# Performance work log

Measured on AMD Instinct MI355X. Metric: run time of the kernel, lower is better.

Reference implementation:

```python
import jax, jax.numpy as jnp
import numpy as np

K = 8
WRM = 40


def _gru(x, h, w_ih, w_hh, b_ih, b_hh):
    # PyTorch GRU cell: gates ordered (r, z, n)
    gi = x @ w_ih.T + b_ih
    gh = h @ w_hh.T + b_hh
    i_r, i_z, i_n = jnp.split(gi, 3, axis=-1)
    h_r, h_z, h_n = jnp.split(gh, 3, axis=-1)
    r = jax.nn.sigmoid(i_r + h_r)
    z = jax.nn.sigmoid(i_z + h_z)
    n = jnp.tanh(i_n + r * h_n)
    return (1.0 - z) * n + z * h


def setup_inputs() -> dict:
    key = jax.random.key(0)
    ks = jax.random.split(key, 20)
    T, B, C, Wd, H = 240, 64, 1, 84, 84
    N, M, E, A = 512, 256, 32, 18
    D = C * Wd * H
    u = lambda k, s, sc: jax.random.uniform(k, s, jnp.float32, -sc, sc)
    sM = float(1.0 / np.sqrt(M))
    sD = float(1.0 / np.sqrt(D))
    return dict(
        obs_seq=jax.random.normal(ks[0], (T, B, C, Wd, H), jnp.float32),
        act_seq=jax.random.randint(ks[1], (T, B), 0, A),
        w_enc=u(ks[2], (N, D), sD), b_enc=u(ks[3], (N,), sD),
        w_ih=u(ks[4], (3 * M, N), sM), w_hh=u(ks[5], (3 * M, M), sM),
        b_ih=u(ks[6], (3 * M,), sM), b_hh=u(ks[7], (3 * M,), sM),
        w_ih_c=u(ks[8], (3 * M, E), sM), w_hh_c=u(ks[9], (3 * M, M), sM),
        b_ih_c=u(ks[10], (3 * M,), sM), b_hh_c=u(ks[11], (3 * M,), sM),
        W1=u(ks[12], (M, M), sM), b1=u(ks[13], (M,), sM),
        W2=u(ks[14], (N, M), sM), b2=u(ks[15], (N,), sM),
        emb=jax.random.normal(ks[16], (A, E), jnp.float32),
    )


def reference(obs_seq, act_seq, w_enc, b_enc, w_ih, w_hh, b_ih, b_hh,
              w_ih_c, w_hh_c, b_ih_c, b_hh_c, W1, b1, W2, b2, emb):
    T, B = obs_seq.shape[0], obs_seq.shape[1]
    M = w_hh.shape[1]
    # encoder: flatten + linear -> (T, B, N)
    z = obs_seq.reshape(T, B, -1) @ w_enc.T + b_enc
    wrm_seq, trn_seq = z[:WRM], z[WRM:]
    acts = act_seq[WRM:]

    h0 = jnp.zeros((B, M), z.dtype)
    warm_hn, _ = jax.lax.scan(
        lambda h, x: (_gru(x, h, w_ih, w_hh, b_ih, b_hh), None), h0, wrm_seq)
    warm_hn = jax.lax.stop_gradient(warm_hn)  # torch.no_grad() warmup

    def cls_step(h, x):
        h2 = _gru(x, h, w_ih, w_hh, b_ih, b_hh)
        return h2, h2

    _, bts = jax.lax.scan(cls_step, warm_hn, trn_seq)  # (T', B, M)

    Tp = bts.shape[0]
    Tout = Tp - K
    idx = jnp.arange(Tout)[:, None] + jnp.arange(K)[None, :]  # (Tout, K)
    act_win = emb[acts[idx]]  # (Tout, K, B, E)

    def open_step(h, x):  # h: (Tout, B, M), x: (Tout, B, E)
        h2 = _gru(x, h, w_ih_c, w_hh_c, b_ih_c, b_hh_c)
        zt = jax.nn.relu(h2 @ W1.T + b1) @ W2.T + b2
        return h2, zt

    _, zs = jax.lax.scan(open_step, bts[:Tout], jnp.transpose(act_win, (1, 0, 2, 3)))
    return jnp.transpose(zs, (1, 0, 2, 3))  # (Tout, K, B, N)
```

## Files before the change

kernel.cpp:

```cpp
#include <hip/hip_runtime.h>
#include <hip/hip_fp16.h>
#include <math.h>

#define TT   240
#define BBATCH 64
#define DDIM 7056
#define KENC_PAD 7072
#define NENC 512
#define MHID 256
#define G3   768
#define WRMC 40
#define KWIN 8
#define TOUTC 192
#define RROWS (TOUTC*BBATCH)
#define NSTEPS (WRMC + TOUTC)

#define B_GI     ((size_t)0)
#define B_WENCH  ((size_t)0)
#define B_GBH    ((size_t)0)
#define B_R1H    ((size_t)37748736)
#define B_ZH     ((size_t)45613056)
#define B_HOPEN  ((size_t)45613056)
#define B_BTS    ((size_t)60817408)
#define B_BTSH   ((size_t)73400320)
#define B_HOPENH ((size_t)79691776)
#define B_WIHH   ((size_t)85983232)
#define B_WHHCH  ((size_t)86769664)
#define B_W1H    ((size_t)87162880)
#define B_W2H    ((size_t)87293952)
#define B_GTAB   ((size_t)87556096)
#define B_WT8    ((size_t)87611392)

typedef _Float16 half8 __attribute__((ext_vector_type(8)));
typedef _Float16 h2v  __attribute__((ext_vector_type(2)));
typedef __attribute__((ext_vector_type(4))) float f32x4;

__device__ __forceinline__ float sigmf(float x) { return 1.0f / (1.0f + expf(-x)); }
__device__ __forceinline__ h2v u2h2(unsigned int u) {
  union { unsigned int u; h2v h; } c; c.u = u; return c.h;
}

__global__ void wconv_kernel(const float* __restrict__ W, __half* __restrict__ o,
                             int N, int K, int Kpad) {
  const int idx = blockIdx.x * 256 + threadIdx.x;
  if (idx >= N * Kpad) return;
  const int n = idx / Kpad, k = idx % Kpad;
  o[idx] = __float2half((k < K) ? W[(size_t)n * K + k] : 0.f);
}

__global__ __launch_bounds__(256, 4) void gemm_h(
    const void* __restrict__ A, int a_fp32, const __half* __restrict__ W,
    const float* __restrict__ bias, void* __restrict__ C,
    int M, int N, int K, int Kpad, int relu, int out_h, int outk)
{
  __shared__ __half Ah[64][40];
  __shared__ __half Bh[256][40];
  const int tid = threadIdx.x;
  const int bx = blockIdx.x, by = blockIdx.y;
  const int w = tid >> 6;
  const int lane = tid & 63;
  const int l15 = lane & 15;
  const int khalf = (lane >> 4) * 8;

  f32x4 acc[4][4];
#pragma unroll
  for (int i = 0; i < 4; ++i)
#pragma unroll
    for (int j = 0; j < 4; ++j) acc[i][j] = (f32x4){0.f, 0.f, 0.f, 0.f};

  const int arow = tid >> 2;
  const int akq = (tid & 3) * 8;

  for (int k0 = 0; k0 < Kpad; k0 += 32) {
    __syncthreads();
    if (a_fp32) {
      const float* Af = (const float*)A;
      float4 v0 = make_float4(0.f, 0.f, 0.f, 0.f);
      float4 v1 = make_float4(0.f, 0.f, 0.f, 0.f);
      const size_t base = (size_t)(by * 64 + arow) * K + k0 + akq;
      if (k0 + akq < K)     v0 = *(const float4*)(Af + base);
      if (k0 + akq + 4 < K) v1 = *(const float4*)(Af + base + 4);
      __half2 hh[4];
      hh[0] = __floats2half2_rn(v0.x, v0.y);
      hh[1] = __floats2half2_rn(v0.z, v0.w);
      hh[2] = __floats2half2_rn(v1.x, v1.y);
      hh[3] = __floats2half2_rn(v1.z, v1.w);
      *(float4*)&Ah[arow][akq] = *(float4*)hh;
    } else {
      const __half* Ahp = (const __half*)A;
      *(float4*)&Ah[arow][akq] =
          *(const float4*)(Ahp + (size_t)(by * 64 + arow) * Kpad + k0 + akq);
    }
#pragma unroll
    for (int u = 0; u < 4; ++u) {
      const int f = tid + u * 256;
      const int n = f >> 2;
      const int kq8 = (f & 3) * 8;
      *(float4*)&Bh[n][kq8] =
          *(const float4*)(W + (size_t)(bx * 256 + n) * Kpad + k0 + kq8);
    }
    __syncthreads();

    half8 ah[4], bh[4];
#pragma unroll
    for (int i = 0; i < 4; ++i) {
      ah[i] = *(half8*)&Ah[i * 16 + l15][khalf];
      bh[i] = *(half8*)&Bh[w * 64 + i * 16 + l15][khalf];
    }
#pragma unroll
    for (int i = 0; i < 4; ++i)
#pragma unroll
      for (int j = 0; j < 4; ++j)
        acc[i][j] = __builtin_amdgcn_mfma_f32_16x16x32_f16(ah[i], bh[j], acc[i][j], 0, 0, 0);
  }

  const int r4 = (lane >> 4) * 4;
#pragma unroll
  for (int j = 0; j < 4; ++j) {
    const int col = bx * 256 + w * 64 + j * 16 + l15;
    const float bc = bias ? bias[col] : 0.f;
#pragma unroll
    for (int i = 0; i < 4; ++i) {
      const int mbase = by * 64 + i * 16 + r4;
#pragma unroll
      for (int r = 0; r < 4; ++r) {
        const int m = mbase + r;
        float vv = acc[i][j][r] + bc;
        if (relu) vv = fmaxf(vv, 0.f);
        if (outk >= 0) {
          const int t = m >> 6, b = m & 63;
          ((float*)C)[(((size_t)(t * KWIN + outk) * BBATCH + b) * NENC) + col] = vv;
        } else if (out_h) {
          ((__half*)C)[(size_t)m * N + col] = __float2half(vv);
        } else {
          ((float*)C)[(size_t)m * N + col] = vv;
        }
      }
    }
  }
}

__global__ void gitab_kernel(const float* __restrict__ emb, const float* __restrict__ w_ih_c,
                             const float* __restrict__ b_ih_c, float* __restrict__ gt)
{
  const int idx = blockIdx.x * blockDim.x + threadIdx.x;
  if (idx >= 18 * G3) return;
  const int a = idx / G3, cgate = idx % G3;
  float s = b_ih_c[cgate];
#pragma unroll
  for (int e = 0; e < 32; ++e) s = fmaf(emb[a * 32 + e], w_ih_c[cgate * 32 + e], s);
  gt[idx] = s;
}

__global__ void transpose_whh_p8(const float* __restrict__ w, float4* __restrict__ wt8) {
  const int id = blockIdx.x * 256 + threadIdx.x;
  if (id >= 32 * G3) return;
  const int k8 = id / G3, j = id % G3;
  const float* src = w + (size_t)j * MHID + k8 * 8;
  __half2 h2[4];
#pragma unroll
  for (int q = 0; q < 4; ++q)
    h2[q] = __floats2half2_rn(src[2 * q], src[2 * q + 1]);
  wt8[id] = *(float4*)h2;
}

__global__ __launch_bounds__(768, 3) void scan4_kernel(
    const float* __restrict__ gi_all, const float4* __restrict__ wt8,
    const float* __restrict__ b_hh, float* __restrict__ bts,
    __half* __restrict__ bts_h)
{
  const int b = blockIdx.x;
  const int j = threadIdx.x;
  __shared__ __align__(16) float hs[256];
  __shared__ __align__(16) __half hs16[256];
  __shared__ float gacc[768];

  unsigned int wreg[128];
#pragma unroll
  for (int k8 = 0; k8 < 32; ++k8) {
    const float4 v = wt8[(size_t)k8 * G3 + j];
    const uint4 u = *(const uint4*)&v;
    wreg[k8 * 4 + 0] = u.x; wreg[k8 * 4 + 1] = u.y;
    wreg[k8 * 4 + 2] = u.z; wreg[k8 * 4 + 3] = u.w;
  }
  const float bj = b_hh[j];
  if (j < 256) { hs[j] = 0.f; hs16[j] = __float2half(0.f); }
  __syncthreads();

  const uint4* h16v = (const uint4*)hs16;

  for (int t = 0; t < NSTEPS; ++t) {
    float gr = 0.f, gz = 0.f, gn = 0.f;
    if (j < 256) {
      const float* gp = gi_all + ((size_t)t * BBATCH + b) * G3;
      gr = gp[j]; gz = gp[256 + j]; gn = gp[512 + j];
    }

    float a0 = bj, a1 = 0.f, a2 = 0.f, a3 = 0.f;
#pragma unroll
    for (int k8 = 0; k8 < 32; ++k8) {
      const uint4 hu = h16v[k8];
#if __has_builtin(__builtin_amdgcn_fdot2)
      a0 = __builtin_amdgcn_fdot2(u2h2(wreg[k8 * 4 + 0]), u2h2(hu.x), a0, false);
      a1 = __builtin_amdgcn_fdot2(u2h2(wreg[k8 * 4 + 1]), u2h2(hu.y), a1, false);
      a2 = __builtin_amdgcn_fdot2(u2h2(wreg[k8 * 4 + 2]), u2h2(hu.z), a2, false);
      a3 = __builtin_amdgcn_fdot2(u2h2(wreg[k8 * 4 + 3]), u2h2(hu.w), a3, false);
#else
      {
        const h2v w0 = u2h2(wreg[k8 * 4 + 0]), w1 = u2h2(wreg[k8 * 4 + 1]);
        const h2v w2 = u2h2(wreg[k8 * 4 + 2]), w3 = u2h2(wreg[k8 * 4 + 3]);
        const h2v x0 = u2h2(hu.x), x1 = u2h2(hu.y), x2 = u2h2(hu.z), x3 = u2h2(hu.w);
        a0 = fmaf((float)w0.x, (float)x0.x, a0); a0 = fmaf((float)w0.y, (float)x0.y, a0);
        a1 = fmaf((float)w1.x, (float)x1.x, a1); a1 = fmaf((float)w1.y, (float)x1.y, a1);
        a2 = fmaf((float)w2.x, (float)x2.x, a2); a2 = fmaf((float)w2.y, (float)x2.y, a2);
        a3 = fmaf((float)w3.x, (float)x3.x, a3); a3 = fmaf((float)w3.y, (float)x3.y, a3);
      }
#endif
    }
    gacc[j] = (a0 + a1) + (a2 + a3);
    __syncthreads();

    if (j < 256) {
      const float r = sigmf(gr + gacc[j]);
      const float z = sigmf(gz + gacc[256 + j]);
      const float n = tanhf(gn + r * gacc[512 + j]);
      const float hn = (1.f - z) * n + z * hs[j];
      hs[j] = hn;
      hs16[j] = __float2half(hn);
      if (t >= WRMC) {
        const size_t o = (((size_t)(t - WRMC)) * BBATCH + b) * MHID + j;
        bts[o] = hn;
        bts_h[o] = __float2half(hn);
      }
    }
    __syncthreads();
  }
}

__global__ __launch_bounds__(256) void open_gates(
    const float* __restrict__ gtab, const int* __restrict__ act_seq,
    const float* __restrict__ gh, const float* __restrict__ hin,
    float* __restrict__ hout, __half* __restrict__ hout_h, int kstep)
{
  const int row = blockIdx.x;
  const int j = threadIdx.x;
  const int t = row >> 6, b = row & 63;
  const int a = act_seq[(WRMC + t + kstep) * BBATCH + b];
  const float* gi = gtab + a * G3;
  const float gr = gi[j], gz = gi[256 + j], gn = gi[512 + j];
  const size_t g0 = (size_t)row * G3;
  const float hr = gh[g0 + j], hz = gh[g0 + 256 + j], hnn = gh[g0 + 512 + j];
  const float h = hin[(size_t)row * MHID + j];
  const float r = sigmf(gr + hr);
  const float z = sigmf(gz + hz);
  const float n = tanhf(gn + r * hnn);
  const float hn = (1.f - z) * n + z * h;
  hout[(size_t)row * MHID + j] = hn;
  hout_h[(size_t)row * MHID + j] = __float2half(hn);
}

extern "C" void kernel_launch(void* const* d_in, const int* in_sizes, int n_in,
                              void* d_out, int out_size, void* d_ws, size_t ws_size,
                              hipStream_t stream) {
  const float* obs    = (const float*)d_in[0];
  const int*   act    = (const int*)  d_in[1];
  const float* w_enc  = (const float*)d_in[2];
  const float* b_enc  = (const float*)d_in[3];
  const float* w_ih   = (const float*)d_in[4];
  const float* w_hh   = (const float*)d_in[5];
  const float* b_ih   = (const float*)d_in[6];
  const float* b_hh   = (const float*)d_in[7];
  const float* w_ih_c = (const float*)d_in[8];
  const float* w_hh_c = (const float*)d_in[9];
  const float* b_ih_c = (const float*)d_in[10];
  const float* b_hh_c = (const float*)d_in[11];
  const float* W1     = (const float*)d_in[12];
  const float* b1     = (const float*)d_in[13];
  const float* W2     = (const float*)d_in[14];
  const float* b2     = (const float*)d_in[15];
  const float* emb    = (const float*)d_in[16];

  char* wsb = (char*)d_ws;
  float* out = (float*)d_out;

  float*  gi      = (float*)(wsb + B_GI);
  float*  gbh     = (float*)(wsb + B_GBH);
  __half* r1_h    = (__half*)(wsb + B_R1H);
  __half* z_h     = (__half*)(wsb + B_ZH);
  float*  hopen   = (float*)(wsb + B_HOPEN);
  float*  bts     = (float*)(wsb + B_BTS);
  __half* bts_h   = (__half*)(wsb + B_BTSH);
  __half* hopen_h = (__half*)(wsb + B_HOPENH);
  __half* enc_h   = (__half*)(wsb + B_WENCH);
  __half* ih_h    = (__half*)(wsb + B_WIHH);
  __half* hhc_h   = (__half*)(wsb + B_WHHCH);
  __half* w1_h    = (__half*)(wsb + B_W1H);
  __half* w2_h    = (__half*)(wsb + B_W2H);
  float*  gtab    = (float*)(wsb + B_GTAB);
  float4* wt8     = (float4*)(wsb + B_WT8);

  const dim3 blk(256);

  wconv_kernel<<<(NENC * KENC_PAD + 255) / 256, blk, 0, stream>>>(w_enc, enc_h, NENC, DDIM, KENC_PAD);
  wconv_kernel<<<(G3 * NENC + 255) / 256, blk, 0, stream>>>(w_ih, ih_h, G3, NENC, NENC);
  wconv_kernel<<<(G3 * MHID + 255) / 256, blk, 0, stream>>>(w_hh_c, hhc_h, G3, MHID, MHID);
  wconv_kernel<<<(MHID * MHID + 255) / 256, blk, 0, stream>>>(W1, w1_h, MHID, MHID, MHID);
  wconv_kernel<<<(NENC * MHID + 255) / 256, blk, 0, stream>>>(W2, w2_h, NENC, MHID, MHID);
  gitab_kernel<<<54, 256, 0, stream>>>(emb, w_ih_c, b_ih_c, gtab);
  transpose_whh_p8<<<(32 * G3 + 255) / 256, blk, 0, stream>>>(w_hh, wt8);

  gemm_h<<<dim3(NENC / 256, NSTEPS * BBATCH / 64), blk, 0, stream>>>(
      obs, 1, enc_h, b_enc, z_h, NSTEPS * BBATCH, NENC, DDIM, KENC_PAD, 0, 1, -1);
  gemm_h<<<dim3(G3 / 256, NSTEPS * BBATCH / 64), blk, 0, stream>>>(
      z_h, 0, ih_h, b_ih, gi, NSTEPS * BBATCH, G3, NENC, NENC, 0, 0, -1);

  scan4_kernel<<<BBATCH, 768, 0, stream>>>(gi, wt8, b_hh, bts, bts_h);

  for (int k = 0; k < KWIN; ++k) {
    const __half* hin_h = (k == 0) ? bts_h : hopen_h;
    const float*  hin   = (k == 0) ? bts   : hopen;
    gemm_h<<<dim3(G3 / 256, RROWS / 64), blk, 0, stream>>>(
        hin_h, 0, hhc_h, b_hh_c, gbh, RROWS, G3, MHID, MHID, 0, 0, -1);
    open_gates<<<RROWS, 256, 0, stream>>>(gtab, act, gbh, hin, hopen, hopen_h, k);
    gemm_h<<<dim3(MHID / 256, RROWS / 64), blk, 0, stream>>>(
        hopen_h, 0, w1_h, b1, r1_h, RROWS, MHID, MHID, MHID, 1, 1, -1);
    gemm_h<<<dim3(NENC / 256, RROWS / 64), blk, 0, stream>>>(
        r1_h, 0, w2_h, b2, out, RROWS, NENC, MHID, MHID, 0, 0, k);
  }
}
```

Before: 1.206 ms.

## Double-buffer GEMM tiles with register prefetch and halve N tile width

```diff
diff --git a/kernel.cpp b/kernel.cpp
--- a/kernel.cpp
+++ b/kernel.cpp
@@ -48,76 +48,90 @@
   o[idx] = __float2half((k < K) ? W[(size_t)n * K + k] : 0.f);
 }
 
-__global__ __launch_bounds__(256, 4) void gemm_h(
-    const void* __restrict__ A, int a_fp32, const __half* __restrict__ W,
+template<int AF32>
+__device__ __forceinline__ void load_tile(
+    const void* A, const __half* W, int by, int bx, int K, int Kpad,
+    int arow, int akq, int tid, int it,
+    float4& ra0, float4& ra1, float4& rah, float4& rb0, float4& rb1)
+{
+  const int k0 = it * 32;
+  if (AF32) {
+    const float* Af = (const float*)A;
+    ra0 = make_float4(0.f, 0.f, 0.f, 0.f); ra1 = ra0;
+    const size_t base = (size_t)(by * 64 + arow) * K + k0 + akq;
+    if (k0 + akq < K)     ra0 = *(const float4*)(Af + base);
+    if (k0 + akq + 4 < K) ra1 = *(const float4*)(Af + base + 4);
+  } else {
+    rah = *(const float4*)((const __half*)A + (size_t)(by * 64 + arow) * Kpad + k0 + akq);
+  }
+  const int bn = tid >> 2, bk = (tid & 3) * 8;
+  rb0 = *(const float4*)(W + (size_t)(bx * 128 + bn) * Kpad + k0 + bk);
+  rb1 = *(const float4*)(W + (size_t)(bx * 128 + 64 + bn) * Kpad + k0 + bk);
+}
+
+template<int AF32>
+__global__ __launch_bounds__(256, 4) void gemm_hp(
+    const void* __restrict__ A, const __half* __restrict__ W,
     const float* __restrict__ bias, void* __restrict__ C,
     int M, int N, int K, int Kpad, int relu, int out_h, int outk)
 {
-  __shared__ __half Ah[64][40];
-  __shared__ __half Bh[256][40];
+  __shared__ __half Ah[2][64][40];
+  __shared__ __half Bh[2][128][40];
   const int tid = threadIdx.x;
   const int bx = blockIdx.x, by = blockIdx.y;
   const int w = tid >> 6;
   const int lane = tid & 63;
   const int l15 = lane & 15;
   const int khalf = (lane >> 4) * 8;
-
-  f32x4 acc[4][4];
-#pragma unroll
-  for (int i = 0; i < 4; ++i)
-#pragma unroll
-    for (int j = 0; j < 4; ++j) acc[i][j] = (f32x4){0.f, 0.f, 0.f, 0.f};
-
   const int arow = tid >> 2;
   const int akq = (tid & 3) * 8;
-
-  for (int k0 = 0; k0 < Kpad; k0 += 32) {
+  const int bn = tid >> 2, bk = (tid & 3) * 8;
+
+  f32x4 acc[4][2];
+#pragma unroll
+  for (int i = 0; i < 4; ++i)
+#pragma unroll
+    for (int j = 0; j < 2; ++j) acc[i][j] = (f32x4){0.f, 0.f, 0.f, 0.f};
+
+  const int niter = Kpad / 32;
+  float4 ra0, ra1, rah, rb0, rb1;
+  load_tile<AF32>(A, W, by, bx, K, Kpad, arow, akq, tid, 0, ra0, ra1, rah, rb0, rb1);
+
+  for (int it = 0; it < niter; ++it) {
+    __half (*Ac)[40] = Ah[it & 1];
+    __half (*Bc)[40] = Bh[it & 1];
+    if (AF32) {
+      __half2 hh[4];
+      hh[0] = __floats2half2_rn(ra0.x, ra0.y);
+      hh[1] = __floats2half2_rn(ra0.z, ra0.w);
+      hh[2] = __floats2half2_rn(ra1.x, ra1.y);
+      hh[3] = __floats2half2_rn(ra1.z, ra1.w);
+      *(float4*)&Ac[arow][akq] = *(float4*)hh;
+    } else {
+      *(float4*)&Ac[arow][akq] = rah;
+    }
+    *(float4*)&Bc[bn][bk] = rb0;
+    *(float4*)&Bc[64 + bn][bk] = rb1;
     __syncthreads();
-    if (a_fp32) {
-      const float* Af = (const float*)A;
-      float4 v0 = make_float4(0.f, 0.f, 0.f, 0.f);
-      float4 v1 = make_float4(0.f, 0.f, 0.f, 0.f);
-      const size_t base = (size_t)(by * 64 + arow) * K + k0 + akq;
-      if (k0 + akq < K)     v0 = *(const float4*)(Af + base);
-      if (k0 + akq + 4 < K) v1 = *(const float4*)(Af + base + 4);
-      __half2 hh[4];
-      hh[0] = __floats2half2_rn(v0.x, v0.y);
-      hh[1] = __floats2half2_rn(v0.z, v0.w);
-      hh[2] = __floats2half2_rn(v1.x, v1.y);
-      hh[3] = __floats2half2_rn(v1.z, v1.w);
-      *(float4*)&Ah[arow][akq] = *(float4*)hh;
-    } else {
-      const __half* Ahp = (const __half*)A;
-      *(float4*)&Ah[arow][akq] =
-          *(const float4*)(Ahp + (size_t)(by * 64 + arow) * Kpad + k0 + akq);
-    }
-#pragma unroll
-    for (int u = 0; u < 4; ++u) {
-      const int f = tid + u * 256;
-      const int n = f >> 2;
-      const int kq8 = (f & 3) * 8;
-      *(float4*)&Bh[n][kq8] =
-          *(const float4*)(W + (size_t)(bx * 256 + n) * Kpad + k0 + kq8);
-    }
-    __syncthreads();
-
-    half8 ah[4], bh[4];
-#pragma unroll
-    for (int i = 0; i < 4; ++i) {
-      ah[i] = *(half8*)&Ah[i * 16 + l15][khalf];
-      bh[i] = *(half8*)&Bh[w * 64 + i * 16 + l15][khalf];
-    }
+    if (it + 1 < niter)
+      load_tile<AF32>(A, W, by, bx, K, Kpad, arow, akq, tid, it + 1, ra0, ra1, rah, rb0, rb1);
+
+    half8 ah[4], bh[2];
+#pragma unroll
+    for (int i = 0; i < 4; ++i) ah[i] = *(half8*)&Ac[i * 16 + l15][khalf];
+#pragma unroll
+    for (int j = 0; j < 2; ++j) bh[j] = *(half8*)&Bc[w * 32 + j * 16 + l15][khalf];
 #pragma unroll
     for (int i = 0; i < 4; ++i)
 #pragma unroll
-      for (int j = 0; j < 4; ++j)
+      for (int j = 0; j < 2; ++j)
         acc[i][j] = __builtin_amdgcn_mfma_f32_16x16x32_f16(ah[i], bh[j], acc[i][j], 0, 0, 0);
   }
 
   const int r4 = (lane >> 4) * 4;
 #pragma unroll
-  for (int j = 0; j < 4; ++j) {
-    const int col = bx * 256 + w * 64 + j * 16 + l15;
+  for (int j = 0; j < 2; ++j) {
+    const int col = bx * 128 + w * 32 + j * 16 + l15;
     const float bc = bias ? bias[col] : 0.f;
 #pragma unroll
     for (int i = 0; i < 4; ++i) {
@@ -309,22 +323,22 @@
   gitab_kernel<<<54, 256, 0, stream>>>(emb, w_ih_c, b_ih_c, gtab);
   transpose_whh_p8<<<(32 * G3 + 255) / 256, blk, 0, stream>>>(w_hh, wt8);
 
-  gemm_h<<<dim3(NENC / 256, NSTEPS * BBATCH / 64), blk, 0, stream>>>(
-      obs, 1, enc_h, b_enc, z_h, NSTEPS * BBATCH, NENC, DDIM, KENC_PAD, 0, 1, -1);
-  gemm_h<<<dim3(G3 / 256, NSTEPS * BBATCH / 64), blk, 0, stream>>>(
-      z_h, 0, ih_h, b_ih, gi, NSTEPS * BBATCH, G3, NENC, NENC, 0, 0, -1);
+  gemm_hp<1><<<dim3(NENC / 128, NSTEPS * BBATCH / 64), blk, 0, stream>>>(
+      obs, enc_h, b_enc, z_h, NSTEPS * BBATCH, NENC, DDIM, KENC_PAD, 0, 1, -1);
+  gemm_hp<0><<<dim3(G3 / 128, NSTEPS * BBATCH / 64), blk, 0, stream>>>(
+      z_h, ih_h, b_ih, gi, NSTEPS * BBATCH, G3, NENC, NENC, 0, 0, -1);
 
   scan4_kernel<<<BBATCH, 768, 0, stream>>>(gi, wt8, b_hh, bts, bts_h);
 
   for (int k = 0; k < KWIN; ++k) {
     const __half* hin_h = (k == 0) ? bts_h : hopen_h;
     const float*  hin   = (k == 0) ? bts   : hopen;
-    gemm_h<<<dim3(G3 / 256, RROWS / 64), blk, 0, stream>>>(
-        hin_h, 0, hhc_h, b_hh_c, gbh, RROWS, G3, MHID, MHID, 0, 0, -1);
+    gemm_hp<0><<<dim3(G3 / 128, RROWS / 64), blk, 0, stream>>>(
+        hin_h, hhc_h, b_hh_c, gbh, RROWS, G3, MHID, MHID, 0, 0, -1);
     open_gates<<<RROWS, 256, 0, stream>>>(gtab, act, gbh, hin, hopen, hopen_h, k);
-    gemm_h<<<dim3(MHID / 256, RROWS / 64), blk, 0, stream>>>(
-        hopen_h, 0, w1_h, b1, r1_h, RROWS, MHID, MHID, MHID, 1, 1, -1);
-    gemm_h<<<dim3(NENC / 256, RROWS / 64), blk, 0, stream>>>(
-        r1_h, 0, w2_h, b2, out, RROWS, NENC, MHID, MHID, 0, 0, k);
-  }
-}
+    gemm_hp<0><<<dim3(MHID / 128, RROWS / 64), blk, 0, stream>>>(
+        hopen_h, w1_h, b1, r1_h, RROWS, MHID, MHID, MHID, 1, 1, -1);
+    gemm_hp<0><<<dim3(NENC / 128, RROWS / 64), blk, 0, stream>>>(
+        r1_h, w2_h, b2, out, RROWS, NENC, MHID, MHID, 0, 0, k);
+  }
+}
```

Result: no change. 1.217 ms (+0.9%).

## Double-buffer GEMM shared tiles with register prefetch two stages ahead

Applied to the files above, without the earlier changes.

```diff
diff --git a/kernel.cpp b/kernel.cpp
--- a/kernel.cpp
+++ b/kernel.cpp
@@ -48,71 +48,99 @@
   o[idx] = __float2half((k < K) ? W[(size_t)n * K + k] : 0.f);
 }
 
-__global__ __launch_bounds__(256, 4) void gemm_h(
-    const void* __restrict__ A, int a_fp32, const __half* __restrict__ W,
+template<int AF32>
+__global__ __launch_bounds__(256, 3) void gemm_hp(
+    const void* __restrict__ A, const __half* __restrict__ W,
     const float* __restrict__ bias, void* __restrict__ C,
     int M, int N, int K, int Kpad, int relu, int out_h, int outk)
 {
-  __shared__ __half Ah[64][40];
-  __shared__ __half Bh[256][40];
+  __shared__ __half Ah[2][64][40];
+  __shared__ __half Bh[2][256][40];
   const int tid = threadIdx.x;
   const int bx = blockIdx.x, by = blockIdx.y;
   const int w = tid >> 6;
   const int lane = tid & 63;
   const int l15 = lane & 15;
   const int khalf = (lane >> 4) * 8;
-
-  f32x4 acc[4][4];
-#pragma unroll
-  for (int i = 0; i < 4; ++i)
-#pragma unroll
-    for (int j = 0; j < 4; ++j) acc[i][j] = (f32x4){0.f, 0.f, 0.f, 0.f};
-
   const int arow = tid >> 2;
   const int akq = (tid & 3) * 8;
-
-  for (int k0 = 0; k0 < Kpad; k0 += 32) {
-    __syncthreads();
-    if (a_fp32) {
-      const float* Af = (const float*)A;
-      float4 v0 = make_float4(0.f, 0.f, 0.f, 0.f);
-      float4 v1 = make_float4(0.f, 0.f, 0.f, 0.f);
-      const size_t base = (size_t)(by * 64 + arow) * K + k0 + akq;
-      if (k0 + akq < K)     v0 = *(const float4*)(Af + base);
-      if (k0 + akq + 4 < K) v1 = *(const float4*)(Af + base + 4);
-      __half2 hh[4];
-      hh[0] = __floats2half2_rn(v0.x, v0.y);
-      hh[1] = __floats2half2_rn(v0.z, v0.w);
-      hh[2] = __floats2half2_rn(v1.x, v1.y);
-      hh[3] = __floats2half2_rn(v1.z, v1.w);
-      *(float4*)&Ah[arow][akq] = *(float4*)hh;
-    } else {
-      const __half* Ahp = (const __half*)A;
-      *(float4*)&Ah[arow][akq] =
-          *(const float4*)(Ahp + (size_t)(by * 64 + arow) * Kpad + k0 + akq);
-    }
-#pragma unroll
-    for (int u = 0; u < 4; ++u) {
-      const int f = tid + u * 256;
-      const int n = f >> 2;
-      const int kq8 = (f & 3) * 8;
-      *(float4*)&Bh[n][kq8] =
-          *(const float4*)(W + (size_t)(bx * 256 + n) * Kpad + k0 + kq8);
-    }
-    __syncthreads();
-
-    half8 ah[4], bh[4];
-#pragma unroll
-    for (int i = 0; i < 4; ++i) {
-      ah[i] = *(half8*)&Ah[i * 16 + l15][khalf];
-      bh[i] = *(half8*)&Bh[w * 64 + i * 16 + l15][khalf];
-    }
-#pragma unroll
-    for (int i = 0; i < 4; ++i)
-#pragma unroll
-      for (int j = 0; j < 4; ++j)
-        acc[i][j] = __builtin_amdgcn_mfma_f32_16x16x32_f16(ah[i], bh[j], acc[i][j], 0, 0, 0);
-  }
+  const int bn = tid >> 2, bk = (tid & 3) * 8;
+
+  f32x4 acc[4][4];
+#pragma unroll
+  for (int i = 0; i < 4; ++i)
+#pragma unroll
+    for (int j = 0; j < 4; ++j) acc[i][j] = (f32x4){0.f, 0.f, 0.f, 0.f};
+
+  const int niter = Kpad / 32;
+
+  float4 raA0, raA1, rahA, rbA0, rbA1, rbA2, rbA3;
+  float4 raB0, raB1, rahB, rbB0, rbB1, rbB2, rbB3;
+
+#define LOADT(IT, ra0, ra1, rah, rb0, rb1, rb2, rb3)                              \
+  {                                                                               \
+    const int k0_ = (IT) * 32;                                                    \
+    if (AF32) {                                                                   \
+      const float* Af_ = (const float*)A;                                         \
+      ra0 = make_float4(0.f, 0.f, 0.f, 0.f); ra1 = ra0;                           \
+      const size_t base_ = (size_t)(by * 64 + arow) * K + k0_ + akq;              \
+      if (k0_ + akq < K)     ra0 = *(const float4*)(Af_ + base_);                 \
+      if (k0_ + akq + 4 < K) ra1 = *(const float4*)(Af_ + base_ + 4);             \
+    } else {                                                                      \
+      rah = *(const float4*)((const __half*)A +                                   \
+            (size_t)(by * 64 + arow) * Kpad + k0_ + akq);                         \
+    }                                                                             \
+    rb0 = *(const float4*)(W + (size_t)(bx * 256 + bn      ) * Kpad + k0_ + bk);  \
+    rb1 = *(const float4*)(W + (size_t)(bx * 256 + bn +  64) * Kpad + k0_ + bk);  \
+    rb2 = *(const float4*)(W + (size_t)(bx * 256 + bn + 128) * Kpad + k0_ + bk);  \
+    rb3 = *(const float4*)(W + (size_t)(bx * 256 + bn + 192) * Kpad + k0_ + bk);  \
+  }
+
+#define BODY(IT, ra0, ra1, rah, rb0, rb1, rb2, rb3)                               \
+  {                                                                               \
+    __half (*Ac)[40] = Ah[(IT) & 1];                                              \
+    __half (*Bc)[40] = Bh[(IT) & 1];                                              \
+    if (AF32) {                                                                   \
+      __half2 hh_[4];                                                             \
+      hh_[0] = __floats2half2_rn(ra0.x, ra0.y);                                   \
+      hh_[1] = __floats2half2_rn(ra0.z, ra0.w);                                   \
+      hh_[2] = __floats2half2_rn(ra1.x, ra1.y);                                   \
+      hh_[3] = __floats2half2_rn(ra1.z, ra1.w);                                   \
+      *(float4*)&Ac[arow][akq] = *(float4*)hh_;                                   \
+    } else {                                                                      \
+      *(float4*)&Ac[arow][akq] = rah;                                             \
+    }                                                                             \
+    *(float4*)&Bc[bn      ][bk] = rb0;                                            \
+    *(float4*)&Bc[bn +  64][bk] = rb1;                                            \
+    *(float4*)&Bc[bn + 128][bk] = rb2;                                            \
+    *(float4*)&Bc[bn + 192][bk] = rb3;                                            \
+    __syncthreads();                                                              \
+    if ((IT) + 2 < niter)                                                         \
+      LOADT((IT) + 2, ra0, ra1, rah, rb0, rb1, rb2, rb3);                         \
+    half8 ah_[4], bh_[4];                                                         \
+    _Pragma("unroll")                                                             \
+    for (int i = 0; i < 4; ++i) ah_[i] = *(half8*)&Ac[i * 16 + l15][khalf];       \
+    _Pragma("unroll")                                                             \
+    for (int j = 0; j < 4; ++j) bh_[j] = *(half8*)&Bc[w * 64 + j * 16 + l15][khalf]; \
+    _Pragma("unroll")                                                             \
+    for (int i = 0; i < 4; ++i)                                                   \
+      _Pragma("unroll")                                                           \
+      for (int j = 0; j < 4; ++j)                                                 \
+        acc[i][j] = __builtin_amdgcn_mfma_f32_16x16x32_f16(ah_[i], bh_[j], acc[i][j], 0, 0, 0); \
+  }
+
+  LOADT(0, raA0, raA1, rahA, rbA0, rbA1, rbA2, rbA3);
+  if (niter > 1) LOADT(1, raB0, raB1, rahB, rbB0, rbB1, rbB2, rbB3);
+
+  int it = 0;
+  while (true) {
+    BODY(it, raA0, raA1, rahA, rbA0, rbA1, rbA2, rbA3);
+    ++it; if (it == niter) break;
+    BODY(it, raB0, raB1, rahB, rbB0, rbB1, rbB2, rbB3);
+    ++it; if (it == niter) break;
+  }
+#undef BODY
+#undef LOADT
 
   const int r4 = (lane >> 4) * 4;
 #pragma unroll
@@ -309,22 +337,22 @@
   gitab_kernel<<<54, 256, 0, stream>>>(emb, w_ih_c, b_ih_c, gtab);
   transpose_whh_p8<<<(32 * G3 + 255) / 256, blk, 0, stream>>>(w_hh, wt8);
 
-  gemm_h<<<dim3(NENC / 256, NSTEPS * BBATCH / 64), blk, 0, stream>>>(
-      obs, 1, enc_h, b_enc, z_h, NSTEPS * BBATCH, NENC, DDIM, KENC_PAD, 0, 1, -1);
-  gemm_h<<<dim3(G3 / 256, NSTEPS * BBATCH / 64), blk, 0, stream>>>(
-      z_h, 0, ih_h, b_ih, gi, NSTEPS * BBATCH, G3, NENC, NENC, 0, 0, -1);
+  gemm_hp<1><<<dim3(NENC / 256, NSTEPS * BBATCH / 64), blk, 0, stream>>>(
+      obs, enc_h, b_enc, z_h, NSTEPS * BBATCH, NENC, DDIM, KENC_PAD, 0, 1, -1);
+  gemm_hp<0><<<dim3(G3 / 256, NSTEPS * BBATCH / 64), blk, 0, stream>>>(
+      z_h, ih_h, b_ih, gi, NSTEPS * BBATCH, G3, NENC, NENC, 0, 0, -1);
 
   scan4_kernel<<<BBATCH, 768, 0, stream>>>(gi, wt8, b_hh, bts, bts_h);
 
   for (int k = 0; k < KWIN; ++k) {
     const __half* hin_h = (k == 0) ? bts_h : hopen_h;
     const float*  hin   = (k == 0) ? bts   : hopen;
-    gemm_h<<<dim3(G3 / 256, RROWS / 64), blk, 0, stream>>>(
-        hin_h, 0, hhc_h, b_hh_c, gbh, RROWS, G3, MHID, MHID, 0, 0, -1);
+    gemm_hp<0><<<dim3(G3 / 256, RROWS / 64), blk, 0, stream>>>(
+        hin_h, hhc_h, b_hh_c, gbh, RROWS, G3, MHID, MHID, 0, 0, -1);
     open_gates<<<RROWS, 256, 0, stream>>>(gtab, act, gbh, hin, hopen, hopen_h, k);
-    gemm_h<<<dim3(MHID / 256, RROWS / 64), blk, 0, stream>>>(
-        hopen_h, 0, w1_h, b1, r1_h, RROWS, MHID, MHID, MHID, 1, 1, -1);
-    gemm_h<<<dim3(NENC / 256, RROWS / 64), blk, 0, stream>>>(
-        r1_h, 0, w2_h, b2, out, RROWS, NENC, MHID, MHID, 0, 0, k);
-  }
-}
+    gemm_hp<0><<<dim3(MHID / 256, RROWS / 64), blk, 0, stream>>>(
+        hopen_h, w1_h, b1, r1_h, RROWS, MHID, MHID, MHID, 1, 1, -1);
+    gemm_hp<0><<<dim3(NENC / 256, RROWS / 64), blk, 0, stream>>>(
+        r1_h, w2_h, b2, out, RROWS, NENC, MHID, MHID, 0, 0, k);
+  }
+}
```

Result: faster. 1.104 ms (median of 2 runs) (-8.4%).
